# Kernel optimization log

Measured on AMD Instinct MI355X. Metric: run time of the kernel, lower is better.

The kernel has to match this reference:

```python
import jax, jax.numpy as jnp
import numpy as np

N = 100000      # nodes
E = 3_200_000   # edges
F_IN = 256      # input feature dim
R = 16          # rank_bound (GCN output dim)
D = 128         # embedding_dim (trans output)
B = 16384       # batch of node indices
EPS = 1e-5


def setup_inputs() -> dict:
    key = jax.random.key(0)
    ks = jax.random.split(key, 9)
    x = jax.random.normal(ks[0], (N, F_IN), jnp.float32)
    edge_index = jax.random.randint(ks[1], (2, E), 0, N, dtype=jnp.int64)
    trans = jax.random.normal(ks[2], (R, D), jnp.float32) * 0.1
    batch = jax.random.randint(ks[3], (B,), 0, N, dtype=jnp.int64)
    W = jax.random.normal(ks[4], (R, F_IN), jnp.float32) / np.sqrt(F_IN).astype(np.float32)
    b = jnp.zeros((R,), jnp.float32)
    ln_w = jnp.ones((R,), jnp.float32)
    ln_b = jnp.zeros((R,), jnp.float32)
    prelu_a = jnp.full((1,), 0.25, jnp.float32)  # PReLU single shared slope
    return dict(x=x, edge_index=edge_index, trans=trans, batch=batch,
                W=W, b=b, ln_w=ln_w, ln_b=ln_b, prelu_a=prelu_a)


def gcn_conv(x, edge_index, W, b):
    # PyG GCNConv: lin first, then symmetric-normalized aggregation with self-loops.
    h = x @ W.T  # [N, R]
    loop = jnp.arange(N, dtype=edge_index.dtype)
    src = jnp.concatenate([edge_index[0], loop])  # messages flow src -> dst
    dst = jnp.concatenate([edge_index[1], loop])
    deg = jax.ops.segment_sum(jnp.ones_like(dst, h.dtype), dst, num_segments=N)
    dinv = jnp.where(deg > 0, jax.lax.rsqrt(deg), 0.0)
    norm = dinv[src] * dinv[dst]                   # [E+N]
    msg = h[src] * norm[:, None]                   # gather [E+N, R]
    out = jax.ops.segment_sum(msg, dst, num_segments=N)  # scatter-add
    return out + b


def reference(x, edge_index, trans, batch, W, b, ln_w, ln_b, prelu_a):
    h = gcn_conv(x, edge_index, W, b)              # [N, R]
    # PyG LayerNorm (graph mode): normalize over all nodes and channels.
    h = h - h.mean()
    var = (h * h).mean()
    h = h * jax.lax.rsqrt(var + EPS) * ln_w + ln_b
    # PReLU
    h = jnp.where(h >= 0, h, prelu_a * h)
    emb = h @ trans                                # [N, D]
    return emb[batch]                              # index_select(0, batch)
```

## Files before the change

kernel.cpp:

```cpp
#include <hip/hip_runtime.h>

#define EPS 1e-5f
#define BSHIFT 8
#define BSIZE  256
#define NBMAX  512
#define PCHUNK 8192
#define BCAP   16384
#define LCAP   12288

typedef short bf16x8 __attribute__((ext_vector_type(8)));
typedef float f32x4  __attribute__((ext_vector_type(4)));

__device__ __forceinline__ unsigned short f2bf(float f) {
    unsigned u = __float_as_uint(f);
    u += 0x7FFFu + ((u >> 16) & 1u);
    return (unsigned short)(u >> 16);
}
__device__ __forceinline__ float bf2f(unsigned short s) {
    return __uint_as_float(((unsigned)s) << 16);
}
__device__ __forceinline__ void acc8(float* acc, uint4 v) {
    acc[0] += bf2f((unsigned short)(v.x & 0xFFFFu)); acc[1] += bf2f((unsigned short)(v.x >> 16));
    acc[2] += bf2f((unsigned short)(v.y & 0xFFFFu)); acc[3] += bf2f((unsigned short)(v.y >> 16));
    acc[4] += bf2f((unsigned short)(v.z & 0xFFFFu)); acc[5] += bf2f((unsigned short)(v.z >> 16));
    acc[6] += bf2f((unsigned short)(v.w & 0xFFFFu)); acc[7] += bf2f((unsigned short)(v.w >> 16));
}
__device__ __forceinline__ void cvt_hilo(const float* f, bf16x8& hi, bf16x8& lo) {
#pragma unroll
    for (int j = 0; j < 8; j++) {
        unsigned short h = f2bf(f[j]);
        hi[j] = (short)h;
        lo[j] = (short)f2bf(f[j] - bf2f(h));
    }
}

__global__ __launch_bounds__(512) void k_init(unsigned* __restrict__ cursor, int NB) {
    int t = threadIdx.x;
    if (t < NB) cursor[t] = (unsigned)t * BCAP;
}

__global__ __launch_bounds__(512) void k_bpart(const int* __restrict__ ei,
                                               unsigned* __restrict__ cursor,
                                               unsigned* __restrict__ sorted, int E, int NB) {
    __shared__ unsigned cnt[NBMAX];
    __shared__ unsigned lbase[NBMAX];
    __shared__ unsigned loff[NBMAX + 1];
    __shared__ unsigned sh[512];
    __shared__ unsigned stage[PCHUNK];
    __shared__ unsigned short bkt[PCHUNK];
    int t = threadIdx.x;
    for (int i = t; i < NB; i += 512) cnt[i] = 0u;
    __syncthreads();
    const int4* src4 = (const int4*)ei;
    const int4* dst4 = (const int4*)(ei + E);
    int E4 = E >> 2;
    int base4 = blockIdx.x * (PCHUNK / 4);
    unsigned rpack[PCHUNK / 4 / 512 * 2];
#pragma unroll
    for (int i = 0; i < PCHUNK / 4 / 512; i++) {
        int idx = base4 + i * 512 + t;
        unsigned r0 = 0, r1 = 0, r2 = 0, r3 = 0;
        if (idx < E4) {
            int4 d = dst4[idx];
            r0 = atomicAdd(&cnt[d.x >> BSHIFT], 1u);
            r1 = atomicAdd(&cnt[d.y >> BSHIFT], 1u);
            r2 = atomicAdd(&cnt[d.z >> BSHIFT], 1u);
            r3 = atomicAdd(&cnt[d.w >> BSHIFT], 1u);
        }
        rpack[2 * i]     = r0 | (r1 << 16);
        rpack[2 * i + 1] = r2 | (r3 << 16);
    }
    __syncthreads();
    unsigned v = (t < NB) ? cnt[t] : 0u;
    sh[t] = v;
    if (t < NB) lbase[t] = v ? atomicAdd(&cursor[t], v) : 0u;
    __syncthreads();
    for (int off = 1; off < 512; off <<= 1) {
        unsigned a = (t >= off) ? sh[t - off] : 0u;
        __syncthreads();
        sh[t] += a;
        __syncthreads();
    }
    if (t < NB) loff[t] = sh[t] - v;
    if (t == NB - 1) loff[NB] = sh[t];
    __syncthreads();
    for (int b = t; b < NB; b += 512) {
        unsigned s = loff[b], e2 = loff[b + 1];
        for (unsigned j = s; j < e2; j++) bkt[j] = (unsigned short)b;
    }
#pragma unroll
    for (int i = 0; i < PCHUNK / 4 / 512; i++) {
        int idx = base4 + i * 512 + t;
        if (idx < E4) {
            int4 s = src4[idx];
            int4 d = dst4[idx];
            unsigned p0 = rpack[2 * i], p1 = rpack[2 * i + 1];
            int b;
            b = d.x >> BSHIFT;
            stage[loff[b] + (p0 & 0xFFFFu)] = (unsigned)s.x | ((unsigned)(d.x & (BSIZE - 1)) << 17);
            b = d.y >> BSHIFT;
            stage[loff[b] + (p0 >> 16)]     = (unsigned)s.y | ((unsigned)(d.y & (BSIZE - 1)) << 17);
            b = d.z >> BSHIFT;
            stage[loff[b] + (p1 & 0xFFFFu)] = (unsigned)s.z | ((unsigned)(d.z & (BSIZE - 1)) << 17);
            b = d.w >> BSHIFT;
            stage[loff[b] + (p1 >> 16)]     = (unsigned)s.w | ((unsigned)(d.w & (BSIZE - 1)) << 17);
        }
    }
    __syncthreads();
    unsigned total = loff[NB];
    for (unsigned i = t; i < total; i += 512) {
        unsigned b = bkt[i];
        sorted[lbase[b] + (i - loff[b])] = stage[i];
    }
}

__global__ __launch_bounds__(512) void k_bdeg(const unsigned* __restrict__ cursor,
                                              const unsigned* __restrict__ sorted,
                                              unsigned* __restrict__ deg, int N) {
    __shared__ unsigned dcnt[BSIZE];
    int b = blockIdx.x, t = threadIdx.x;
    if (t < BSIZE) dcnt[t] = 0u;
    __syncthreads();
    unsigned s0 = (unsigned)b * BCAP, s1 = cursor[b];
    for (unsigned j = s0 + t; j < s1; j += 512)
        atomicAdd(&dcnt[sorted[j] >> 17], 1u);
    __syncthreads();
    if (t < BSIZE) {
        int node = (b << BSHIFT) + t;
        if (node < N) deg[node] = dcnt[t];
    }
}

__global__ __launch_bounds__(256, 4) void k_gemm(const float* __restrict__ x,
                                                 const float* __restrict__ W,
                                                 const unsigned* __restrict__ deg,
                                                 unsigned short* __restrict__ hs,
                                                 int N, int NT) {
    int t = threadIdx.x;
    int w = t >> 6, lane = t & 63;
    int lr = lane & 15;
    int lk = lane >> 4;
    bf16x8 bh[8], bl[8];
#pragma unroll
    for (int kt = 0; kt < 8; kt++) {
        float wf[8];
        const float* wp = W + lr * 256 + kt * 32 + lk * 8;
        *(float4*)&wf[0] = *(const float4*)wp;
        *(float4*)&wf[4] = *(const float4*)(wp + 4);
        cvt_hilo(wf, bh[kt], bl[kt]);
    }
    int nw = gridDim.x * 4;
    int wid = blockIdx.x * 4 + w;
    for (int tile = wid; tile < NT; tile += nw) {
        int nb = tile << 4;
        int node = nb + lr;
        const float* xp = x + (size_t)node * 256;
        f32x4 acc = {0.f, 0.f, 0.f, 0.f};
#pragma unroll
        for (int kt = 0; kt < 8; kt++) {
            float af[8];
            if (node < N) {
                const float* ap = xp + kt * 32 + lk * 8;
                *(float4*)&af[0] = *(const float4*)ap;
                *(float4*)&af[4] = *(const float4*)(ap + 4);
            } else {
#pragma unroll
                for (int j = 0; j < 8; j++) af[j] = 0.f;
            }
            bf16x8 ah, al;
            cvt_hilo(af, ah, al);
            acc = __builtin_amdgcn_mfma_f32_16x16x32_bf16(ah, bh[kt], acc, 0, 0, 0);
            acc = __builtin_amdgcn_mfma_f32_16x16x32_bf16(al, bh[kt], acc, 0, 0, 0);
            acc = __builtin_amdgcn_mfma_f32_16x16x32_bf16(ah, bl[kt], acc, 0, 0, 0);
        }
#pragma unroll
        for (int i = 0; i < 4; i++) {
            int n2 = nb + lk * 4 + i;
            if (n2 < N) {
                float dv = rsqrtf((float)(deg[n2] + 1u));
                hs[(size_t)n2 * 16 + lr] = f2bf(acc[i] * dv);
            }
        }
    }
}

__global__ __launch_bounds__(512) void k_aggf(const unsigned* __restrict__ cursor,
                                              const unsigned* __restrict__ deg,
                                              const unsigned* __restrict__ sorted,
                                              const unsigned short* __restrict__ hs,
                                              const float* __restrict__ bias,
                                              float* __restrict__ agg,
                                              float2* __restrict__ part,
                                              unsigned* __restrict__ scratch, int N) {
    __shared__ unsigned buf[LCAP];
    __shared__ unsigned cur0[BSIZE + 1];
    __shared__ unsigned curv[BSIZE];
    __shared__ float dnv[BSIZE];
    __shared__ unsigned wsum[4];
    __shared__ float ss[8], qq[8];
    int b = blockIdx.x, t = threadIdx.x;
    unsigned s0 = (unsigned)b * BCAP, s1 = cursor[b];
    unsigned len = s1 - s0;
    unsigned d0 = 0, inc = 0;
    int lane = t & 63, wv = t >> 6;
    if (t < BSIZE) {
        int node = (b << BSHIFT) + t;
        d0 = (node < N) ? deg[node] : 0u;
        dnv[t] = rsqrtf((float)(d0 + 1u));
        inc = d0;
        for (int off = 1; off < 64; off <<= 1) {
            unsigned u = __shfl_up(inc, off, 64);
            if (lane >= off) inc += u;
        }
        if (lane == 63) wsum[wv] = inc;
    }
    __syncthreads();
    if (t < BSIZE) {
        unsigned wbase = 0;
        for (int w = 0; w < wv; w++) wbase += wsum[w];
        unsigned excl = wbase + inc - d0;
        cur0[t] = excl;
        curv[t] = excl;
    }
    if (t == 0) cur0[BSIZE] = len;
    __syncthreads();
    bool fit = (len <= (unsigned)LCAP);
    if (fit) {
        for (unsigned j = t; j < len; j += 512) {
            unsigned u = sorted[s0 + j];
            unsigned pos = atomicAdd(&curv[u >> 17], 1u);
            buf[pos] = u & 0x1FFFFu;
        }
    } else {
        for (unsigned j = t; j < len; j += 512) {
            unsigned u = sorted[s0 + j];
            unsigned pos = atomicAdd(&curv[u >> 17], 1u);
            scratch[s0 + pos] = u & 0x1FFFFu;
        }
    }
    __syncthreads();
    int g = t >> 4, r = t & 15;
    int sub = r >> 1;
    int half = r & 1;
    float sacc = 0.f, qacc = 0.f;
#pragma unroll 1
    for (int p = 0; p < 8; p++) {
        int dloc = p * 32 + g;
        int d = (b << BSHIFT) + dloc;
        float acc[8];
#pragma unroll
        for (int c = 0; c < 8; c++) acc[c] = 0.f;
        if (d < N) {
            unsigned l0 = cur0[dloc], l1 = cur0[dloc + 1];
            for (unsigned j = l0; j < l1; j += 16) {
                unsigned row0 = j + sub, row1 = j + 8 + sub;
                bool p0 = row0 < l1, p1 = row1 < l1;
                unsigned i0 = 0, i1 = 0;
                if (fit) {
                    if (p0) i0 = buf[row0];
                    if (p1) i1 = buf[row1];
                } else {
                    if (p0) i0 = scratch[s0 + row0];
                    if (p1) i1 = scratch[s0 + row1];
                }
                uint4 v0, v1;
                if (p0) v0 = ((const uint4*)(hs + (size_t)i0 * 16))[half];
                if (p1) v1 = ((const uint4*)(hs + (size_t)i1 * 16))[half];
                if (p0) acc8(acc, v0);
                if (p1) acc8(acc, v1);
            }
        }
#pragma unroll
        for (int off = 2; off <= 8; off <<= 1) {
#pragma unroll
            for (int c = 0; c < 8; c++) acc[c] += __shfl_down(acc[c], off, 64);
        }
        if (d < N && r < 2) {
            float dd = dnv[dloc];
            uint4 hv = ((const uint4*)(hs + (size_t)d * 16))[half];
            float self[8];
            self[0] = bf2f((unsigned short)(hv.x & 0xFFFFu)); self[1] = bf2f((unsigned short)(hv.x >> 16));
            self[2] = bf2f((unsigned short)(hv.y & 0xFFFFu)); self[3] = bf2f((unsigned short)(hv.y >> 16));
            self[4] = bf2f((unsigned short)(hv.z & 0xFFFFu)); self[5] = bf2f((unsigned short)(hv.z >> 16));
            self[6] = bf2f((unsigned short)(hv.w & 0xFFFFu)); self[7] = bf2f((unsigned short)(hv.w >> 16));
            float o[8];
#pragma unroll
            for (int c = 0; c < 8; c++) o[c] = (acc[c] + self[c]) * dd;
            float* an = agg + (size_t)d * 16 + half * 8;
            *(float4*)(an)     = make_float4(o[0], o[1], o[2], o[3]);
            *(float4*)(an + 4) = make_float4(o[4], o[5], o[6], o[7]);
            const float* bp = bias + half * 8;
            float4 b0 = *(const float4*)bp, b1 = *(const float4*)(bp + 4);
            float a0 = o[0] + b0.x, a1 = o[1] + b0.y, a2 = o[2] + b0.z, a3 = o[3] + b0.w;
            float a4 = o[4] + b1.x, a5 = o[5] + b1.y, a6 = o[6] + b1.z, a7 = o[7] + b1.w;
            sacc += (a0 + a1) + (a2 + a3) + (a4 + a5) + (a6 + a7);
            qacc += a0 * a0 + a1 * a1 + a2 * a2 + a3 * a3 + a4 * a4 + a5 * a5 + a6 * a6 + a7 * a7;
        }
    }
    for (int off = 32; off > 0; off >>= 1) {
        sacc += __shfl_down(sacc, off, 64);
        qacc += __shfl_down(qacc, off, 64);
    }
    if (lane == 0) { ss[wv] = sacc; qq[wv] = qacc; }
    __syncthreads();
    if (t == 0) {
        float s = 0.f, q = 0.f;
#pragma unroll
        for (int i = 0; i < 8; i++) { s += ss[i]; q += qq[i]; }
        part[b] = make_float2(s, q);
    }
}

__global__ __launch_bounds__(256) void k_final(const float* __restrict__ agg,
                                               const int* __restrict__ batch,
                                               const float* __restrict__ trans,
                                               const float* __restrict__ bias,
                                               const float* __restrict__ ln_w,
                                               const float* __restrict__ ln_b,
                                               const float* __restrict__ prelu_a,
                                               const float2* __restrict__ part,
                                               float* __restrict__ out, int B, float invCnt, int M) {
    __shared__ float tl[16 * 128];
    __shared__ float hh[8 * 16];
    __shared__ float ssr[4], qqr[4];
    const int tid = threadIdx.x;
    for (int i = tid; i < 2048; i += 256) tl[i] = trans[i];
    float s = 0.f, q = 0.f;
    for (int i = tid; i < M; i += 256) {
        float2 v = part[i];
        s += v.x; q += v.y;
    }
    for (int off = 32; off > 0; off >>= 1) {
        s += __shfl_down(s, off, 64);
        q += __shfl_down(q, off, 64);
    }
    int lane = tid & 63, wd = tid >> 6;
    if (lane == 0) { ssr[wd] = s; qqr[wd] = q; }
    __syncthreads();
    float S = ssr[0] + ssr[1] + ssr[2] + ssr[3];
    float Q = qqr[0] + qqr[1] + qqr[2] + qqr[3];
    float mean = S * invCnt;
    float var  = Q * invCnt - mean * mean;
    float inv  = rsqrtf(var + EPS);
    int row0 = blockIdx.x * 8;
    if (tid < 128) {
        int lr = tid >> 4, r = tid & 15;
        int row = row0 + lr;
        if (row < B) {
            int node = batch[row];
            float v = agg[(size_t)node * 16 + r] + bias[r];
            v = (v - mean) * inv * ln_w[r] + ln_b[r];
            float a = prelu_a[0];
            v = v >= 0.f ? v : a * v;
            hh[lr * 16 + r] = v;
        }
    }
    __syncthreads();
    int d = tid & 127, hlf = tid >> 7;
    float tv[16];
#pragma unroll
    for (int r = 0; r < 16; r++) tv[r] = tl[r * 128 + d];
#pragma unroll
    for (int rr = 0; rr < 4; rr++) {
        int lr = rr * 2 + hlf;
        int row = row0 + lr;
        if (row < B) {
            const float* hrow = hh + lr * 16;
            float acc = 0.f;
#pragma unroll
            for (int r = 0; r < 16; r++) acc += hrow[r] * tv[r];
            out[(size_t)row * 128 + d] = acc;
        }
    }
}

extern "C" void kernel_launch(void* const* d_in, const int* in_sizes, int n_in,
                              void* d_out, int out_size, void* d_ws, size_t ws_size,
                              hipStream_t stream) {
    const float* x       = (const float*)d_in[0];
    const int*   ei      = (const int*)d_in[1];
    const float* trans   = (const float*)d_in[2];
    const int*   batch   = (const int*)d_in[3];
    const float* W       = (const float*)d_in[4];
    const float* bias    = (const float*)d_in[5];
    const float* ln_w    = (const float*)d_in[6];
    const float* ln_b    = (const float*)d_in[7];
    const float* prelu_a = (const float*)d_in[8];
    float* out = (float*)d_out;

    const int N = in_sizes[0] / 256;
    const int E = in_sizes[1] / 2;
    const int B = in_sizes[3];
    const int NB = (N + BSIZE - 1) >> BSHIFT;
    const int pbp = (E + PCHUNK - 1) / PCHUNK;
    const int NT = (N + 15) / 16;

    char* p = (char*)d_ws;
    unsigned short* hs = (unsigned short*)p;  p += (size_t)N * 16 * 2;
    float*    agg     = (float*)p;     p += (size_t)N * 16 * 4;
    unsigned* sorted  = (unsigned*)p;  p += (size_t)NB * BCAP * 4;
    unsigned* scratch = (unsigned*)p;  p += (size_t)NB * BCAP * 4;
    unsigned* deg     = (unsigned*)p;  p += (size_t)N * 4;
    unsigned* cursor  = (unsigned*)p;  p += NBMAX * 4;
    p = (char*)(((size_t)p + 7) & ~(size_t)7);
    float2*   part    = (float2*)p;    p += (size_t)NB * 8;

    hipLaunchKernelGGL(k_init,  dim3(1),           dim3(512), 0, stream, cursor, NB);
    hipLaunchKernelGGL(k_bpart, dim3(pbp),         dim3(512), 0, stream, ei, cursor, sorted, E, NB);
    hipLaunchKernelGGL(k_bdeg,  dim3(NB),          dim3(512), 0, stream, cursor, sorted, deg, N);
    hipLaunchKernelGGL(k_gemm,  dim3(512),         dim3(256), 0, stream, x, W, deg, hs, N, NT);
    hipLaunchKernelGGL(k_aggf,  dim3(NB),          dim3(512), 0, stream, cursor, deg, sorted, hs, bias, agg, part, scratch, N);
    hipLaunchKernelGGL(k_final, dim3((B + 7) / 8), dim3(256), 0, stream, agg, batch, trans, bias,
                       ln_w, ln_b, prelu_a, part, out, B, 1.0f / (float)(N * 16), NB);
}
```

Baseline: 260.0 us.

## Split each aggregation bucket across two blocks handling half the destinations

Each 256-node destination bucket in the fused aggregation kernel is now handled by two workgroups, each owning 128 destinations. Each block still scans the whole bucket's edge list but keeps only the edges for its half, so it needs half the LDS and does half the gather work. The grid doubles (~391 to ~782 blocks) to fill more CUs and raise occupancy. The cost is reading the bucket's sorted edge list twice, and the partial-stats count passed to the final kernel doubles accordingly.

```diff
diff --git a/kernel.cpp b/kernel.cpp
--- a/kernel.cpp
+++ b/kernel.cpp
@@ -6,7 +6,7 @@
 #define NBMAX  512
 #define PCHUNK 8192
 #define BCAP   16384
-#define LCAP   12288
+#define LCAP2  6144
 
 typedef short bf16x8 __attribute__((ext_vector_type(8)));
 typedef float f32x4  __attribute__((ext_vector_type(4)));
@@ -192,19 +192,21 @@
                                               float* __restrict__ agg,
                                               float2* __restrict__ part,
                                               unsigned* __restrict__ scratch, int N) {
-    __shared__ unsigned buf[LCAP];
-    __shared__ unsigned cur0[BSIZE + 1];
-    __shared__ unsigned curv[BSIZE];
-    __shared__ float dnv[BSIZE];
-    __shared__ unsigned wsum[4];
+    __shared__ unsigned buf[LCAP2];
+    __shared__ unsigned cur0[129];
+    __shared__ unsigned curv[128];
+    __shared__ float dnv[128];
+    __shared__ unsigned wsum[2];
     __shared__ float ss[8], qq[8];
-    int b = blockIdx.x, t = threadIdx.x;
+    int bb = blockIdx.x;
+    int b = bb >> 1, hr = bb & 1;
+    int t = threadIdx.x;
     unsigned s0 = (unsigned)b * BCAP, s1 = cursor[b];
     unsigned len = s1 - s0;
     unsigned d0 = 0, inc = 0;
     int lane = t & 63, wv = t >> 6;
-    if (t < BSIZE) {
-        int node = (b << BSHIFT) + t;
+    if (t < 128) {
+        int node = (b << BSHIFT) + hr * 128 + t;
         d0 = (node < N) ? deg[node] : 0u;
         dnv[t] = rsqrtf((float)(d0 + 1u));
         inc = d0;
@@ -215,27 +217,34 @@
         if (lane == 63) wsum[wv] = inc;
     }
     __syncthreads();
-    if (t < BSIZE) {
-        unsigned wbase = 0;
-        for (int w = 0; w < wv; w++) wbase += wsum[w];
+    unsigned ownedLen = wsum[0] + wsum[1];
+    if (t < 128) {
+        unsigned wbase = (wv == 1) ? wsum[0] : 0u;
         unsigned excl = wbase + inc - d0;
         cur0[t] = excl;
         curv[t] = excl;
     }
-    if (t == 0) cur0[BSIZE] = len;
-    __syncthreads();
-    bool fit = (len <= (unsigned)LCAP);
+    if (t == 0) cur0[128] = ownedLen;
+    __syncthreads();
+    bool fit = (ownedLen <= (unsigned)LCAP2);
+    unsigned sbase = s0 + (unsigned)hr * (BCAP / 2);
     if (fit) {
         for (unsigned j = t; j < len; j += 512) {
             unsigned u = sorted[s0 + j];
-            unsigned pos = atomicAdd(&curv[u >> 17], 1u);
-            buf[pos] = u & 0x1FFFFu;
+            unsigned dl = u >> 17;
+            if ((int)(dl >> 7) == hr) {
+                unsigned pos = atomicAdd(&curv[dl & 127], 1u);
+                buf[pos] = u & 0x1FFFFu;
+            }
         }
     } else {
         for (unsigned j = t; j < len; j += 512) {
             unsigned u = sorted[s0 + j];
-            unsigned pos = atomicAdd(&curv[u >> 17], 1u);
-            scratch[s0 + pos] = u & 0x1FFFFu;
+            unsigned dl = u >> 17;
+            if ((int)(dl >> 7) == hr) {
+                unsigned pos = atomicAdd(&curv[dl & 127], 1u);
+                scratch[sbase + pos] = u & 0x1FFFFu;
+            }
         }
     }
     __syncthreads();
@@ -244,9 +253,9 @@
     int half = r & 1;
     float sacc = 0.f, qacc = 0.f;
 #pragma unroll 1
-    for (int p = 0; p < 8; p++) {
+    for (int p = 0; p < 4; p++) {
         int dloc = p * 32 + g;
-        int d = (b << BSHIFT) + dloc;
+        int d = (b << BSHIFT) + hr * 128 + dloc;
         float acc[8];
 #pragma unroll
         for (int c = 0; c < 8; c++) acc[c] = 0.f;
@@ -260,8 +269,8 @@
                     if (p0) i0 = buf[row0];
                     if (p1) i1 = buf[row1];
                 } else {
-                    if (p0) i0 = scratch[s0 + row0];
-                    if (p1) i1 = scratch[s0 + row1];
+                    if (p0) i0 = scratch[sbase + row0];
+                    if (p1) i1 = scratch[sbase + row1];
                 }
                 uint4 v0, v1;
                 if (p0) v0 = ((const uint4*)(hs + (size_t)i0 * 16))[half];
@@ -307,7 +316,7 @@
         float s = 0.f, q = 0.f;
 #pragma unroll
         for (int i = 0; i < 8; i++) { s += ss[i]; q += qq[i]; }
-        part[b] = make_float2(s, q);
+        part[bb] = make_float2(s, q);
     }
 }
 
@@ -403,13 +412,13 @@
     unsigned* deg     = (unsigned*)p;  p += (size_t)N * 4;
     unsigned* cursor  = (unsigned*)p;  p += NBMAX * 4;
     p = (char*)(((size_t)p + 7) & ~(size_t)7);
-    float2*   part    = (float2*)p;    p += (size_t)NB * 8;
+    float2*   part    = (float2*)p;    p += (size_t)NB * 2 * 8;
 
     hipLaunchKernelGGL(k_init,  dim3(1),           dim3(512), 0, stream, cursor, NB);
     hipLaunchKernelGGL(k_bpart, dim3(pbp),         dim3(512), 0, stream, ei, cursor, sorted, E, NB);
     hipLaunchKernelGGL(k_bdeg,  dim3(NB),          dim3(512), 0, stream, cursor, sorted, deg, N);
     hipLaunchKernelGGL(k_gemm,  dim3(512),         dim3(256), 0, stream, x, W, deg, hs, N, NT);
-    hipLaunchKernelGGL(k_aggf,  dim3(NB),          dim3(512), 0, stream, cursor, deg, sorted, hs, bias, agg, part, scratch, N);
+    hipLaunchKernelGGL(k_aggf,  dim3(NB * 2),      dim3(512), 0, stream, cursor, deg, sorted, hs, bias, agg, part, scratch, N);
     hipLaunchKernelGGL(k_final, dim3((B + 7) / 8), dim3(256), 0, stream, agg, batch, trans, bias,
-                       ln_w, ln_b, prelu_a, part, out, B, 1.0f / (float)(N * 16), NB);
-}
+                       ln_w, ln_b, prelu_a, part, out, B, 1.0f / (float)(N * 16), NB * 2);
+}
```

Measured after the change: 266.5 us. +2.5%, slower.
